# Kernel tuning notes

Hardware: AMD Instinct MI355X
Metric: run time of the kernel (lower is better)

Reference implementation:

```python
import jax, jax.numpy as jnp
import numpy as np

DIM = 512
INNER = 512  # heads*dim_head = 8*64
SCALE = 64 ** -0.5  # dim_head^{-0.5}, applied to BOTH q and k as in the source


def setup_inputs() -> dict:
    key = jax.random.key(0)
    k1, k2, k3, k4 = jax.random.split(key, 4)
    x = jax.random.normal(k1, (8, 2048, DIM), dtype=jnp.float32)
    Wqkv = jax.random.normal(k2, (DIM, 3 * INNER), dtype=jnp.float32) * (DIM ** -0.5)
    Wout = jax.random.normal(k3, (INNER, DIM), dtype=jnp.float32) * (INNER ** -0.5)
    bout = jax.random.normal(k4, (DIM,), dtype=jnp.float32) * 0.01
    return {"x": x, "Wqkv": Wqkv, "Wout": Wout, "bout": bout}


def reference(x, Wqkv, Wout, bout):
    # fused QKV projection (no bias)
    qkv = jnp.einsum("bnd,de->bne", x, Wqkv)
    q, k, v = jnp.split(qkv, 3, axis=-1)
    # note: source scales BOTH q and k by dim_head^{-0.5}
    scores = jnp.einsum("bnd,bmd->bnm", q * SCALE, k * SCALE)  # [B,N,N]
    attn = jax.nn.softmax(scores, axis=-1)
    out = jnp.einsum("bnm,bmd->bnd", attn, v)
    # residual add, then output projection (dropout=0.0 -> identity)
    return jnp.einsum("bnd,de->bne", out + x, Wout) + bout
```

## Files before the change

### kernel.cpp

```cpp
#include <hip/hip_runtime.h>
#include <hip/hip_bf16.h>


typedef __attribute__((ext_vector_type(8))) short bf16x8;
typedef __attribute__((ext_vector_type(4))) float f32x4;

__device__ __forceinline__ unsigned short f2bf(float f) {
  unsigned u = __builtin_bit_cast(unsigned, f);
  u += 0x7fffu + ((u >> 16) & 1u);
  return (unsigned short)(u >> 16);
}
__device__ __forceinline__ float bf2f(unsigned short h) {
  unsigned u = ((unsigned)h) << 16;
  return __builtin_bit_cast(float, u);
}

__device__ __forceinline__ void async16(const unsigned short* g, unsigned short* l) {
  __builtin_amdgcn_global_load_lds(
      (const __attribute__((address_space(1))) unsigned int*)g,
      (__attribute__((address_space(3))) unsigned int*)l, 16, 0, 0);
}

__global__ __launch_bounds__(256) void prep_x(const float* __restrict__ X,
                                              unsigned short* __restrict__ XB) {
  const size_t base = ((size_t)blockIdx.x * 256 + threadIdx.x) * 16;
  f32x4 a0 = *(const f32x4*)&X[base];
  f32x4 a1 = *(const f32x4*)&X[base + 4];
  f32x4 a2 = *(const f32x4*)&X[base + 8];
  f32x4 a3 = *(const f32x4*)&X[base + 12];
  bf16x8 o0, o1;
#pragma unroll
  for (int j = 0; j < 4; ++j) {
    o0[j] = (short)f2bf(a0[j]);
    o0[4 + j] = (short)f2bf(a1[j]);
    o1[j] = (short)f2bf(a2[j]);
    o1[4 + j] = (short)f2bf(a3[j]);
  }
  *(bf16x8*)&XB[base] = o0;
  *(bf16x8*)&XB[base + 8] = o1;
}

__global__ __launch_bounds__(256) void prep_w(const float* __restrict__ W,
                                              unsigned short* __restrict__ WT) {
  const int t = threadIdx.x;
  const int c0 = blockIdx.x * 128 + (t & 15) * 8;
  const int k0 = blockIdx.y * 128 + (t >> 4) * 8;
  float r[8][8];
#pragma unroll
  for (int j = 0; j < 8; ++j) {
    f32x4 lo = *(const f32x4*)&W[(size_t)(k0 + j) * 1536 + c0];
    f32x4 hi = *(const f32x4*)&W[(size_t)(k0 + j) * 1536 + c0 + 4];
#pragma unroll
    for (int q = 0; q < 4; ++q) {
      r[j][q] = lo[q];
      r[j][4 + q] = hi[q];
    }
  }
#pragma unroll
  for (int i = 0; i < 8; ++i) {
    const float scl = (c0 + i < 1024) ? 0.125f : 1.0f;
    bf16x8 o;
#pragma unroll
    for (int j = 0; j < 8; ++j) o[j] = (short)f2bf(r[j][i] * scl);
    *(bf16x8*)&WT[(size_t)(c0 + i) * 512 + k0] = o;
  }
}

__global__ __launch_bounds__(256) void transpose_wout(const float* __restrict__ W,
                                                      unsigned short* __restrict__ WT) {
  const int t = threadIdx.x;
  const int c0 = blockIdx.x * 128 + (t & 15) * 8;
  const int k0 = blockIdx.y * 128 + (t >> 4) * 8;
  float r[8][8];
#pragma unroll
  for (int j = 0; j < 8; ++j) {
    f32x4 lo = *(const f32x4*)&W[(size_t)(k0 + j) * 512 + c0];
    f32x4 hi = *(const f32x4*)&W[(size_t)(k0 + j) * 512 + c0 + 4];
#pragma unroll
    for (int q = 0; q < 4; ++q) {
      r[j][q] = lo[q];
      r[j][4 + q] = hi[q];
    }
  }
#pragma unroll
  for (int i = 0; i < 8; ++i) {
    bf16x8 o;
#pragma unroll
    for (int j = 0; j < 8; ++j) o[j] = (short)f2bf(r[j][i]);
    *(bf16x8*)&WT[(size_t)(c0 + i) * 512 + k0] = o;
  }
}

__global__ __launch_bounds__(256) void transpose_v(const unsigned short* __restrict__ QKV,
                                                   unsigned short* __restrict__ VT) {
  const int t = threadIdx.x;
  const int m0 = blockIdx.x * 128 + (t & 15) * 8;
  const int d0 = blockIdx.y * 128 + (t >> 4) * 8;
  bf16x8 r[8];
#pragma unroll
  for (int j = 0; j < 8; ++j)
    r[j] = *(const bf16x8*)&QKV[(size_t)(m0 + j) * 1536 + 1024 + d0];
#pragma unroll
  for (int i = 0; i < 8; ++i) {
    bf16x8 o;
#pragma unroll
    for (int j = 0; j < 8; ++j) o[j] = r[j][i];
    *(bf16x8*)&VT[(size_t)(d0 + i) * 16384 + m0] = o;
  }
}


#define GEMM97_VARS                                            \
  const int tid = threadIdx.x;                                 \
  const int wave = tid >> 6, lane = tid & 63;                  \
  const int wr = wave >> 1, wc = wave & 1;                     \
  const int lg = lane >> 4, ll = lane & 15;                    \
  const int kk = lg * 8;                                       \
  const int srow = wave * 32 + (lane >> 2);                    \
  const int scol = (lane & 3) * 8;

#define GEMM97DB_BODY(AG, ASTR, BG, BSTR, KDIM)                                          \
  __shared__ __align__(16) unsigned short Asm[2][4096];                                  \
  __shared__ __align__(16) unsigned short Bsm[2][4096];                                  \
  GEMM97_VARS                                                                            \
  f32x4 acc[4][4];                                                                       \
  _Pragma("unroll") for (int i = 0; i < 4; ++i) _Pragma("unroll") for (int j = 0; j < 4; \
                                                                       ++j) acc[i][j] =  \
      (f32x4){0.f, 0.f, 0.f, 0.f};                                                       \
  async16(&AG[(size_t)srow * ASTR + scol], &Asm[0][wave * 1024]);                        \
  async16(&AG[(size_t)(srow + 16) * ASTR + scol], &Asm[0][wave * 1024 + 512]);           \
  async16(&BG[(size_t)srow * BSTR + scol], &Bsm[0][wave * 1024]);                        \
  async16(&BG[(size_t)(srow + 16) * BSTR + scol], &Bsm[0][wave * 1024 + 512]);           \
  int cur = 0;                                                                           \
  for (int kt = 0; kt < KDIM; kt += 32) {                                                \
    __syncthreads();                                                                     \
    if (kt + 32 < KDIM) {                                                                \
      async16(&AG[(size_t)srow * ASTR + kt + 32 + scol], &Asm[cur ^ 1][wave * 1024]);    \
      async16(&AG[(size_t)(srow + 16) * ASTR + kt + 32 + scol],                          \
              &Asm[cur ^ 1][wave * 1024 + 512]);                                         \
      async16(&BG[(size_t)srow * BSTR + kt + 32 + scol], &Bsm[cur ^ 1][wave * 1024]);    \
      async16(&BG[(size_t)(srow + 16) * BSTR + kt + 32 + scol],                          \
              &Bsm[cur ^ 1][wave * 1024 + 512]);                                         \
    }                                                                                    \
    bf16x8 af[4], bfr[4];                                                                \
    _Pragma("unroll") for (int ai = 0; ai < 4; ++ai) af[ai] =                            \
        *(const bf16x8*)&Asm[cur][(wr * 64 + ai * 16 + ll) * 32 + kk];                   \
    _Pragma("unroll") for (int bj = 0; bj < 4; ++bj) bfr[bj] =                           \
        *(const bf16x8*)&Bsm[cur][(wc * 64 + bj * 16 + ll) * 32 + kk];                   \
    _Pragma("unroll") for (int ai = 0; ai < 4; ++ai) _Pragma("unroll") for (int bj = 0;  \
                                                                            bj < 4;      \
                                                                            ++bj)        \
        acc[ai][bj] =                                                                    \
        __builtin_amdgcn_mfma_f32_16x16x32_bf16(af[ai], bfr[bj], acc[ai][bj], 0, 0, 0);  \
    cur ^= 1;                                                                            \
  }

__global__ __launch_bounds__(256, 3) void gemm_qkv97(const unsigned short* __restrict__ XB,
                                                     const unsigned short* __restrict__ WT,
                                                     unsigned short* __restrict__ QKV) {
  const int bid = blockIdx.x;
  const int qt = bid / 12, nt = bid - qt * 12;
  const unsigned short* Ag = XB + (size_t)(qt * 128) * 512;
  const unsigned short* Bg = WT + (size_t)(nt * 128) * 512;
  GEMM97DB_BODY(Ag, 512, Bg, 512, 512)
#pragma unroll
  for (int ai = 0; ai < 4; ++ai)
#pragma unroll
    for (int bj = 0; bj < 4; ++bj) {
      const int col = nt * 128 + wc * 64 + bj * 16 + ll;
#pragma unroll
      for (int r = 0; r < 4; ++r) {
        const int row = qt * 128 + wr * 64 + ai * 16 + lg * 4 + r;
        QKV[(size_t)row * 1536 + col] = f2bf(acc[ai][bj][r]);
      }
    }
}

__global__ __launch_bounds__(256, 3) void sgemm97(const unsigned short* __restrict__ QKV,
                                                  unsigned short* __restrict__ S,
                                                  float* __restrict__ part) {
  const int bid = blockIdx.x;
  const int b = bid & 7;
  const int idx = bid >> 3;
  const int kvt = idx & 15, qt = idx >> 4;
  const unsigned short* Ag = QKV + ((size_t)b * 2048 + qt * 128) * 1536;
  const unsigned short* Bg = QKV + ((size_t)b * 2048 + kvt * 128) * 1536 + 512;
  GEMM97DB_BODY(Ag, 1536, Bg, 1536, 512)

#pragma unroll
  for (int ai = 0; ai < 4; ++ai)
#pragma unroll
    for (int bj = 0; bj < 4; ++bj)
#pragma unroll
      for (int r = 0; r < 4; ++r) acc[ai][bj][r] = __expf(acc[ai][bj][r]);

  __syncthreads();
  float* sc = (float*)&Asm[0][0];
#pragma unroll
  for (int ai = 0; ai < 4; ++ai)
#pragma unroll
    for (int r = 0; r < 4; ++r) {
      float se = (acc[ai][0][r] + acc[ai][1][r]) + (acc[ai][2][r] + acc[ai][3][r]);
      se += __shfl_xor(se, 1);
      se += __shfl_xor(se, 2);
      se += __shfl_xor(se, 4);
      se += __shfl_xor(se, 8);
      if (ll == 0) sc[wave * 64 + ai * 16 + lg * 4 + r] = se;
    }
  __syncthreads();
  if (tid < 128) {
    const int wrr = tid >> 6, rl = tid & 63;
    const float l = sc[(wrr * 2 + 0) * 64 + rl] + sc[(wrr * 2 + 1) * 64 + rl];
    part[(size_t)(b * 2048 + qt * 128 + tid) * 16 + kvt] = l;
  }

  unsigned short* Sg = S + (size_t)b * 2048 * 2048;
#pragma unroll
  for (int ai = 0; ai < 4; ++ai)
#pragma unroll
    for (int bj = 0; bj < 4; ++bj) {
      const int col = kvt * 128 + wc * 64 + bj * 16 + ll;
#pragma unroll
      for (int r = 0; r < 4; ++r) {
        const int row = qt * 128 + wr * 64 + ai * 16 + lg * 4 + r;
        Sg[(size_t)row * 2048 + col] = f2bf(acc[ai][bj][r]);
      }
    }
}

__global__ __launch_bounds__(256) void combine_l(const float* __restrict__ part,
                                                 float* __restrict__ invl) {
  const int row = blockIdx.x * 256 + threadIdx.x;
  float l = 0.f;
#pragma unroll
  for (int t = 0; t < 16; ++t) l += part[(size_t)row * 16 + t];
  invl[row] = 1.0f / l;
}

__global__ __launch_bounds__(256, 3) void pvgemm97(const unsigned short* __restrict__ S,
                                                   const unsigned short* __restrict__ VT,
                                                   const float* __restrict__ X,
                                                   const float* __restrict__ invl,
                                                   unsigned short* __restrict__ RES) {
  const int bid = blockIdx.x;
  const int b = bid & 7;
  const int idx = bid >> 3;
  const int dt = idx & 3, qt = idx >> 2;
  const unsigned short* Ag = S + (size_t)b * 2048 * 2048 + (size_t)(qt * 128) * 2048;
  const unsigned short* Bg = VT + (size_t)(dt * 128) * 16384 + (size_t)b * 2048;
  GEMM97DB_BODY(Ag, 2048, Bg, 16384, 2048)

  const int rowbase = b * 2048 + qt * 128 + wr * 64;
  float il[4][4];
#pragma unroll
  for (int ai = 0; ai < 4; ++ai)
#pragma unroll
    for (int r = 0; r < 4; ++r) il[ai][r] = invl[rowbase + ai * 16 + lg * 4 + r];
#pragma unroll
  for (int ai = 0; ai < 4; ++ai)
#pragma unroll
    for (int bj = 0; bj < 4; ++bj) {
      const int col = dt * 128 + wc * 64 + bj * 16 + ll;
#pragma unroll
      for (int r = 0; r < 4; ++r) {
        const size_t row = (size_t)rowbase + ai * 16 + lg * 4 + r;
        const float val = acc[ai][bj][r] * il[ai][r] + X[row * 512 + col];
        RES[row * 1536 + 1024 + col] = f2bf(val);
      }
    }
}

__global__ __launch_bounds__(256, 3) void gemm_out97(const unsigned short* __restrict__ A,
                                                     const unsigned short* __restrict__ WT,
                                                     const float* __restrict__ bias,
                                                     float* __restrict__ OUT) {
  const int bid = blockIdx.x;
  const int dt = bid & 3, qt = bid >> 2;
  const unsigned short* Ag = A + (size_t)(qt * 128) * 1536 + 1024;
  const unsigned short* Bg = WT + (size_t)(dt * 128) * 512;
  GEMM97DB_BODY(Ag, 1536, Bg, 512, 512)
#pragma unroll
  for (int ai = 0; ai < 4; ++ai)
#pragma unroll
    for (int bj = 0; bj < 4; ++bj) {
      const int col = dt * 128 + wc * 64 + bj * 16 + ll;
      const float bv = bias[col];
#pragma unroll
      for (int r = 0; r < 4; ++r) {
        const int row = qt * 128 + wr * 64 + ai * 16 + lg * 4 + r;
        OUT[(size_t)row * 512 + col] = acc[ai][bj][r] + bv;
      }
    }
}

extern "C" void kernel_launch(void* const* d_in, const int* in_sizes, int n_in,
                              void* d_out, int out_size, void* d_ws, size_t ws_size,
                              hipStream_t stream) {
  const float* x = (const float*)d_in[0];
  const float* Wqkv = (const float*)d_in[1];
  const float* Wout = (const float*)d_in[2];
  const float* bout = (const float*)d_in[3];
  float* out = (float*)d_out;

  unsigned short* qkvb = (unsigned short*)d_ws;
  unsigned short* VT = qkvb + (size_t)16384 * 1536;
  unsigned short* S = VT + (size_t)512 * 16384;
  unsigned short* xb = S;
  unsigned short* WT = S + (size_t)16384 * 512;
  unsigned short* WoutT = VT;
  float* part = out;
  float* invl = out + (size_t)16384 * 16;

  prep_x<<<2048, 256, 0, stream>>>(x, xb);
  prep_w<<<dim3(12, 4), 256, 0, stream>>>(Wqkv, WT);
  gemm_qkv97<<<1536, 256, 0, stream>>>(xb, WT, qkvb);
  transpose_v<<<dim3(128, 4), 256, 0, stream>>>(qkvb, VT);
  sgemm97<<<2048, 256, 0, stream>>>(qkvb, S, part);
  combine_l<<<64, 256, 0, stream>>>(part, invl);
  pvgemm97<<<512, 256, 0, stream>>>(S, VT, x, invl, qkvb);
  transpose_wout<<<dim3(4, 4), 256, 0, stream>>>(Wout, WoutT);
  gemm_out97<<<512, 256, 0, stream>>>(qkvb, WoutT, bout, out);
}
```

Before: 193.3 us.

## Replace double-buffered GEMM loop with single-buffer, widen PV k-tile to 64

Removes the LDS double buffering from the shared GEMM macro, going back to a load-sync-compute-sync loop on one 32-wide k tile. The PV GEMM gets its own loop with 64-wide k tiles, halving the barrier count over its 2048-long reduction. The S GEMM writes per-wave row-sum partials straight to global memory instead of reducing them through LDS with extra barriers, and combine_l now sums 32 partials with vector loads. This gives up overlap of the next tile's loads with compute in exchange for less LDS use and fewer synchronisations.

```diff
diff --git a/kernel.cpp b/kernel.cpp
--- a/kernel.cpp
+++ b/kernel.cpp
@@ -119,40 +119,31 @@
   const int srow = wave * 32 + (lane >> 2);                    \
   const int scol = (lane & 3) * 8;
 
-#define GEMM97DB_BODY(AG, ASTR, BG, BSTR, KDIM)                                          \
-  __shared__ __align__(16) unsigned short Asm[2][4096];                                  \
-  __shared__ __align__(16) unsigned short Bsm[2][4096];                                  \
+#define GEMM97_BODY(AG, ASTR, BG, BSTR, KDIM)                                            \
+  __shared__ __align__(16) unsigned short Asm[4096];                                     \
+  __shared__ __align__(16) unsigned short Bsm[4096];                                     \
   GEMM97_VARS                                                                            \
   f32x4 acc[4][4];                                                                       \
   _Pragma("unroll") for (int i = 0; i < 4; ++i) _Pragma("unroll") for (int j = 0; j < 4; \
                                                                        ++j) acc[i][j] =  \
       (f32x4){0.f, 0.f, 0.f, 0.f};                                                       \
-  async16(&AG[(size_t)srow * ASTR + scol], &Asm[0][wave * 1024]);                        \
-  async16(&AG[(size_t)(srow + 16) * ASTR + scol], &Asm[0][wave * 1024 + 512]);           \
-  async16(&BG[(size_t)srow * BSTR + scol], &Bsm[0][wave * 1024]);                        \
-  async16(&BG[(size_t)(srow + 16) * BSTR + scol], &Bsm[0][wave * 1024 + 512]);           \
-  int cur = 0;                                                                           \
   for (int kt = 0; kt < KDIM; kt += 32) {                                                \
+    async16(&AG[(size_t)srow * ASTR + kt + scol], &Asm[wave * 1024]);                    \
+    async16(&AG[(size_t)(srow + 16) * ASTR + kt + scol], &Asm[wave * 1024 + 512]);       \
+    async16(&BG[(size_t)srow * BSTR + kt + scol], &Bsm[wave * 1024]);                    \
+    async16(&BG[(size_t)(srow + 16) * BSTR + kt + scol], &Bsm[wave * 1024 + 512]);       \
     __syncthreads();                                                                     \
-    if (kt + 32 < KDIM) {                                                                \
-      async16(&AG[(size_t)srow * ASTR + kt + 32 + scol], &Asm[cur ^ 1][wave * 1024]);    \
-      async16(&AG[(size_t)(srow + 16) * ASTR + kt + 32 + scol],                          \
-              &Asm[cur ^ 1][wave * 1024 + 512]);                                         \
-      async16(&BG[(size_t)srow * BSTR + kt + 32 + scol], &Bsm[cur ^ 1][wave * 1024]);    \
-      async16(&BG[(size_t)(srow + 16) * BSTR + kt + 32 + scol],                          \
-              &Bsm[cur ^ 1][wave * 1024 + 512]);                                         \
-    }                                                                                    \
     bf16x8 af[4], bfr[4];                                                                \
     _Pragma("unroll") for (int ai = 0; ai < 4; ++ai) af[ai] =                            \
-        *(const bf16x8*)&Asm[cur][(wr * 64 + ai * 16 + ll) * 32 + kk];                   \
+        *(const bf16x8*)&Asm[(wr * 64 + ai * 16 + ll) * 32 + kk];                        \
     _Pragma("unroll") for (int bj = 0; bj < 4; ++bj) bfr[bj] =                           \
-        *(const bf16x8*)&Bsm[cur][(wc * 64 + bj * 16 + ll) * 32 + kk];                   \
+        *(const bf16x8*)&Bsm[(wc * 64 + bj * 16 + ll) * 32 + kk];                        \
     _Pragma("unroll") for (int ai = 0; ai < 4; ++ai) _Pragma("unroll") for (int bj = 0;  \
                                                                             bj < 4;      \
                                                                             ++bj)        \
         acc[ai][bj] =                                                                    \
         __builtin_amdgcn_mfma_f32_16x16x32_bf16(af[ai], bfr[bj], acc[ai][bj], 0, 0, 0);  \
-    cur ^= 1;                                                                            \
+    __syncthreads();                                                                     \
   }
 
 __global__ __launch_bounds__(256, 3) void gemm_qkv97(const unsigned short* __restrict__ XB,
@@ -162,7 +153,7 @@
   const int qt = bid / 12, nt = bid - qt * 12;
   const unsigned short* Ag = XB + (size_t)(qt * 128) * 512;
   const unsigned short* Bg = WT + (size_t)(nt * 128) * 512;
-  GEMM97DB_BODY(Ag, 512, Bg, 512, 512)
+  GEMM97_BODY(Ag, 512, Bg, 512, 512)
 #pragma unroll
   for (int ai = 0; ai < 4; ++ai)
 #pragma unroll
@@ -185,7 +176,7 @@
   const int kvt = idx & 15, qt = idx >> 4;
   const unsigned short* Ag = QKV + ((size_t)b * 2048 + qt * 128) * 1536;
   const unsigned short* Bg = QKV + ((size_t)b * 2048 + kvt * 128) * 1536 + 512;
-  GEMM97DB_BODY(Ag, 1536, Bg, 1536, 512)
+  GEMM97_BODY(Ag, 1536, Bg, 1536, 512)
 
 #pragma unroll
   for (int ai = 0; ai < 4; ++ai)
@@ -194,8 +185,6 @@
 #pragma unroll
       for (int r = 0; r < 4; ++r) acc[ai][bj][r] = __expf(acc[ai][bj][r]);
 
-  __syncthreads();
-  float* sc = (float*)&Asm[0][0];
 #pragma unroll
   for (int ai = 0; ai < 4; ++ai)
 #pragma unroll
@@ -205,14 +194,11 @@
       se += __shfl_xor(se, 2);
       se += __shfl_xor(se, 4);
       se += __shfl_xor(se, 8);
-      if (ll == 0) sc[wave * 64 + ai * 16 + lg * 4 + r] = se;
-    }
-  __syncthreads();
-  if (tid < 128) {
-    const int wrr = tid >> 6, rl = tid & 63;
-    const float l = sc[(wrr * 2 + 0) * 64 + rl] + sc[(wrr * 2 + 1) * 64 + rl];
-    part[(size_t)(b * 2048 + qt * 128 + tid) * 16 + kvt] = l;
-  }
+      if (ll == 0) {
+        const size_t rowg = (size_t)b * 2048 + qt * 128 + wr * 64 + ai * 16 + lg * 4 + r;
+        part[rowg * 32 + kvt * 2 + wc] = se;
+      }
+    }
 
   unsigned short* Sg = S + (size_t)b * 2048 * 2048;
 #pragma unroll
@@ -233,7 +219,10 @@
   const int row = blockIdx.x * 256 + threadIdx.x;
   float l = 0.f;
 #pragma unroll
-  for (int t = 0; t < 16; ++t) l += part[(size_t)row * 16 + t];
+  for (int t = 0; t < 8; ++t) {
+    f32x4 v = *(const f32x4*)&part[(size_t)row * 32 + t * 4];
+    l += (v[0] + v[1]) + (v[2] + v[3]);
+  }
   invl[row] = 1.0f / l;
 }
 
@@ -242,13 +231,50 @@
                                                    const float* __restrict__ X,
                                                    const float* __restrict__ invl,
                                                    unsigned short* __restrict__ RES) {
+  __shared__ __align__(16) unsigned short Asm[8192];
+  __shared__ __align__(16) unsigned short Bsm[8192];
+  const int tid = threadIdx.x;
+  const int wave = tid >> 6, lane = tid & 63;
+  const int wr = wave >> 1, wc = wave & 1;
+  const int lg = lane >> 4, ll = lane & 15;
   const int bid = blockIdx.x;
   const int b = bid & 7;
   const int idx = bid >> 3;
   const int dt = idx & 3, qt = idx >> 2;
   const unsigned short* Ag = S + (size_t)b * 2048 * 2048 + (size_t)(qt * 128) * 2048;
   const unsigned short* Bg = VT + (size_t)(dt * 128) * 16384 + (size_t)b * 2048;
-  GEMM97DB_BODY(Ag, 2048, Bg, 16384, 2048)
+  const int s64row = wave * 32 + (lane >> 3);
+  const int s64col = (lane & 7) * 8;
+
+  f32x4 acc[4][4];
+#pragma unroll
+  for (int i = 0; i < 4; ++i)
+#pragma unroll
+    for (int j = 0; j < 4; ++j) acc[i][j] = (f32x4){0.f, 0.f, 0.f, 0.f};
+
+  for (int kt = 0; kt < 2048; kt += 64) {
+#pragma unroll
+    for (int i = 0; i < 4; ++i) {
+      async16(&Ag[(size_t)(s64row + i * 8) * 2048 + kt + s64col], &Asm[wave * 2048 + i * 512]);
+      async16(&Bg[(size_t)(s64row + i * 8) * 16384 + kt + s64col], &Bsm[wave * 2048 + i * 512]);
+    }
+    __syncthreads();
+#pragma unroll
+    for (int half = 0; half < 2; ++half) {
+      const int kk64 = half * 32 + lg * 8;
+      bf16x8 af[4], bfr[4];
+#pragma unroll
+      for (int ai = 0; ai < 4; ++ai) af[ai] = *(const bf16x8*)&Asm[(wr * 64 + ai * 16 + ll) * 64 + kk64];
+#pragma unroll
+      for (int bj = 0; bj < 4; ++bj) bfr[bj] = *(const bf16x8*)&Bsm[(wc * 64 + bj * 16 + ll) * 64 + kk64];
+#pragma unroll
+      for (int ai = 0; ai < 4; ++ai)
+#pragma unroll
+        for (int bj = 0; bj < 4; ++bj)
+          acc[ai][bj] = __builtin_amdgcn_mfma_f32_16x16x32_bf16(af[ai], bfr[bj], acc[ai][bj], 0, 0, 0);
+    }
+    __syncthreads();
+  }
 
   const int rowbase = b * 2048 + qt * 128 + wr * 64;
   float il[4][4];
@@ -278,7 +304,7 @@
   const int dt = bid & 3, qt = bid >> 2;
   const unsigned short* Ag = A + (size_t)(qt * 128) * 1536 + 1024;
   const unsigned short* Bg = WT + (size_t)(dt * 128) * 512;
-  GEMM97DB_BODY(Ag, 1536, Bg, 512, 512)
+  GEMM97_BODY(Ag, 1536, Bg, 512, 512)
 #pragma unroll
   for (int ai = 0; ai < 4; ++ai)
 #pragma unroll
@@ -309,7 +335,7 @@
   unsigned short* WT = S + (size_t)16384 * 512;
   unsigned short* WoutT = VT;
   float* part = out;
-  float* invl = out + (size_t)16384 * 16;
+  float* invl = out + (size_t)16384 * 32;
 
   prep_x<<<2048, 256, 0, stream>>>(x, xb);
   prep_w<<<dim3(12, 4), 256, 0, stream>>>(Wqkv, WT);
```

After: 195.0 us. No clear change (+0.9%).
